# Performance work log

Hardware: AMD Instinct MI355X
Metric: run time of the kernel (lower is better)

Reference implementation:

```python
import jax, jax.numpy as jnp
import numpy as np

B, C, H, W = 16, 512, 64, 64
K = 4            # num_experts
D = C // 16      # reduction=16 -> hidden channels 32


def setup_inputs() -> dict:
    key = jax.random.key(0)
    ks = jax.random.split(key, 7)
    s_fc = 1.0 / np.sqrt(C)
    s_w1 = 1.0 / np.sqrt(C)   # conv1x1 fan_in = C
    s_w2 = 1.0 / np.sqrt(D)   # conv1x1 fan_in = D
    return {
        "x": jax.random.normal(ks[0], (B, C, H, W), dtype=jnp.float32),
        "fc_w": jax.random.uniform(ks[1], (K, C), minval=-s_fc, maxval=s_fc, dtype=jnp.float32),
        "fc_b": jax.random.uniform(ks[2], (K,), minval=-s_fc, maxval=s_fc, dtype=jnp.float32),
        "w1": jax.random.uniform(ks[3], (K, D, C), minval=-s_w1, maxval=s_w1, dtype=jnp.float32),
        "b1": jax.random.uniform(ks[4], (K, D), minval=-s_w1, maxval=s_w1, dtype=jnp.float32),
        "w2": jax.random.uniform(ks[5], (K, C, D), minval=-s_w2, maxval=s_w2, dtype=jnp.float32),
        "b2": jax.random.uniform(ks[6], (K, C), minval=-s_w2, maxval=s_w2, dtype=jnp.float32),
    }


def reference(x, fc_w, fc_b, w1, b1, w2, b2):
    # global average pool -> routing weights over K experts
    y = jnp.mean(x, axis=(2, 3))                                  # [B, C]
    weights = jax.nn.softmax(y @ fc_w.T + fc_b, axis=1)           # [B, K]
    # all experts' first conv1x1 + ReLU, batched over K
    hid = jax.nn.relu(
        jnp.einsum("bchw,kdc->bkdhw", x, w1) + b1[None, :, :, None, None]
    )                                                             # [B, K, D, H, W]
    # second conv1x1 fused with the weighted sum over experts (avoids [B,K,C,H,W])
    out = jnp.einsum("bkdhw,kcd,bk->bchw", hid, w2, weights)
    out = out + jnp.einsum("bk,kc->bc", weights, b2)[:, :, None, None]
    attn = jax.nn.sigmoid(out)                                    # [B, C, H, W]
    return x * attn
```

## Files before the change

kernel.cpp:

```cpp
#include <hip/hip_runtime.h>
#include <hip/hip_bf16.h>
#include <math.h>

#define BB 16
#define CC 512
#define HWN 4096
#define KK 4
#define DD 32
#define KD 128
#define NPIX 64

typedef __attribute__((ext_vector_type(8))) short short8;
typedef __attribute__((ext_vector_type(4))) float f32x4;

#define WS_Y     0
#define WS_WGT   8192
#define WS_BIAS2 8256
#define WS_W1B   16448
#define WS_W2B   49216

__device__ inline unsigned short f2bf(float f) {
    unsigned u = __builtin_bit_cast(unsigned, f);
    unsigned r = (u + 0x7FFFu + ((u >> 16) & 1u)) >> 16;
    return (unsigned short)r;
}

__global__ __launch_bounds__(256) void mean_kernel(const float* __restrict__ x,
                                                   float* __restrict__ y) {
    int wave = threadIdx.x >> 6;
    int lane = threadIdx.x & 63;
    int row  = blockIdx.x * 4 + wave;
    const float4* xr = (const float4*)(x + (size_t)row * HWN);
    float s = 0.f;
    #pragma unroll
    for (int i = 0; i < 16; i++) {
        float4 v = xr[i * 64 + lane];
        s += (v.x + v.y) + (v.z + v.w);
    }
    #pragma unroll
    for (int off = 32; off > 0; off >>= 1)
        s += __shfl_down(s, off, 64);
    if (lane == 0) y[row] = s * (1.0f / HWN);
}

__global__ __launch_bounds__(64) void route_kernel(const float* __restrict__ y,
                                                   const float* __restrict__ fc_w,
                                                   const float* __restrict__ fc_b,
                                                   float* __restrict__ wgt) {
    __shared__ float logits[BB][KK];
    int t = threadIdx.x;
    int b = t >> 2, k = t & 3;
    const float4* y4 = (const float4*)(y + b * CC);
    const float4* f4 = (const float4*)(fc_w + k * CC);
    float s = fc_b[k];
    for (int i = 0; i < CC / 4; i++) {
        float4 a = y4[i], w = f4[i];
        s += a.x * w.x + a.y * w.y + a.z * w.z + a.w * w.w;
    }
    logits[b][k] = s;
    __syncthreads();
    if (k == 0) {
        float m = logits[b][0];
        #pragma unroll
        for (int j = 1; j < KK; j++) m = fmaxf(m, logits[b][j]);
        float e[KK], sum = 0.f;
        #pragma unroll
        for (int j = 0; j < KK; j++) { e[j] = __expf(logits[b][j] - m); sum += e[j]; }
        float inv = 1.f / sum;
        #pragma unroll
        for (int j = 0; j < KK; j++) wgt[b * KK + j] = e[j] * inv;
    }
}

__global__ __launch_bounds__(256) void prep_kernel(const float* __restrict__ w1,
                                                   const float* __restrict__ w2,
                                                   const float* __restrict__ b2,
                                                   const float* __restrict__ wgt,
                                                   unsigned short* __restrict__ w1b,
                                                   unsigned short* __restrict__ w2b,
                                                   float* __restrict__ bias2) {
    int tid = blockIdx.x * 256 + threadIdx.x;
    int n   = gridDim.x * 256;
    for (int idx = tid; idx < CC * KD; idx += n) {
        int f = idx >> 9, rem = idx & 511;
        int l = rem >> 3, i = rem & 7;
        int ks = f >> 3, m = f & 7;
        int kd = m * 16 + (l & 15);
        int c  = ks * 32 + (l >> 4) * 8 + i;
        w1b[idx] = f2bf(w1[kd * CC + c]);
    }
    for (int idx = tid; idx < CC * KD; idx += n) {
        int f = idx >> 9, rem = idx & 511;
        int l = rem >> 3, i = rem & 7;
        int mc = f >> 2, kk = f & 3;
        int c = mc * 16 + (l & 15);
        int d = (l >> 4) * 8 + i;
        w2b[idx] = f2bf(w2[(kk * CC + c) * DD + d]);
    }
    for (int idx = tid; idx < BB * CC; idx += n) {
        int bb = idx >> 9, c = idx & 511;
        float s = 0.f;
        #pragma unroll
        for (int k = 0; k < KK; k++) s += wgt[bb * KK + k] * b2[k * CC + c];
        bias2[idx] = s;
    }
}

__global__ __launch_bounds__(512, 4) void main_kernel(const float* __restrict__ x,
                                                      const unsigned short* __restrict__ w1b,
                                                      const float* __restrict__ b1,
                                                      const unsigned short* __restrict__ w2b,
                                                      const float* __restrict__ wgt,
                                                      const float* __restrict__ bias2,
                                                      float* __restrict__ out) {
    __shared__ char lds[4 * 8192];

    const int b       = blockIdx.y;
    const int pixbase = blockIdx.x * NPIX;
    const int tid = threadIdx.x;
    const int wv  = tid >> 6;
    const int l   = tid & 63;
    const int l15 = l & 15, lg = l >> 4;
    const int pg  = wv & 3;
    const int kh  = wv >> 2;

    const float* xb = x + (size_t)b * CC * HWN;
    const short8* w1f = (const short8*)w1b;
    const short8* w2f = (const short8*)w2b;

    f32x4 acc1[8];
    #pragma unroll
    for (int m = 0; m < 8; m++) acc1[m] = (f32x4)0.f;

    const int mypix = pixbase + pg * 16 + l15;
    const float* xc = xb + (size_t)(kh * 256 + lg * 8) * HWN + mypix;

    float xv[8];
    #pragma unroll
    for (int i = 0; i < 8; i++) xv[i] = xc[(size_t)i * HWN];

    #pragma unroll
    for (int ks8 = 0; ks8 < 8; ks8++) {
        short8 bf;
        #pragma unroll
        for (int i = 0; i < 8; i++) bf[i] = (short)f2bf(xv[i]);
        if (ks8 < 7) {
            const float* xn = xc + (size_t)((ks8 + 1) * 32) * HWN;
            #pragma unroll
            for (int i = 0; i < 8; i++) xv[i] = xn[(size_t)i * HWN];
        }
        const int ks = kh * 8 + ks8;
        #pragma unroll
        for (int m = 0; m < 8; m++) {
            short8 af = w1f[(ks * 8 + m) * 64 + l];
            acc1[m] = __builtin_amdgcn_mfma_f32_16x16x32_bf16(af, bf, acc1[m], 0, 0, 0);
        }
    }

    if (kh == 1) {
        char* base = lds + pg * 8192 + lg * 256 + l15 * 16;
        #pragma unroll
        for (int m = 0; m < 8; m++)
            *(f32x4*)(base + m * 1024) = acc1[m];
    }
    __syncthreads();

    if (kh == 0) {
        const char* pbase = lds + pg * 8192 + lg * 256 + l15 * 16;
        #pragma unroll
        for (int half = 0; half < 2; half++) {
            f32x4 pp[4];
            #pragma unroll
            for (int m4 = 0; m4 < 4; m4++)
                pp[m4] = *(const f32x4*)(pbase + (half * 4 + m4) * 1024);
            #pragma unroll
            for (int m4 = 0; m4 < 4; m4++) {
                const int m = half * 4 + m4;
                f32x4 bv = *(const f32x4*)(b1 + m * 16 + lg * 4);
                float wk = wgt[b * KK + (m >> 1)];
                f32x4 s = acc1[m] + pp[m4];
                unsigned short h[4];
                #pragma unroll
                for (int r = 0; r < 4; r++) {
                    float t = fmaxf(s[r] + bv[r], 0.f) * wk;
                    h[r] = f2bf(t);
                }
                unsigned lo = (unsigned)h[0] | ((unsigned)h[1] << 16);
                unsigned hi = (unsigned)h[2] | ((unsigned)h[3] << 16);
                int byteoff = pg * 8192 + l15 * 256 + (m * 16 + lg * 4) * 2;
                byteoff ^= (l15 & 7) << 4;
                uint2 v; v.x = lo; v.y = hi;
                *(uint2*)(lds + byteoff) = v;
            }
        }
    }
    __syncthreads();

    const float* bb2 = bias2 + b * CC;
    #pragma unroll
    for (int mblk = 0; mblk < 4; mblk++) {
        f32x4 acc[4];
        #pragma unroll
        for (int nb = 0; nb < 4; nb++) acc[nb] = (f32x4)0.f;
        #pragma unroll
        for (int kk = 0; kk < 4; kk++) {
            short8 af = w2f[((wv * 4 + mblk) * 4 + kk) * 64 + l];
            #pragma unroll
            for (int nb = 0; nb < 4; nb++) {
                int byteoff = nb * 8192 + l15 * 256 + kk * 64 + lg * 16;
                byteoff ^= (l15 & 7) << 4;
                short8 bf = *(const short8*)(lds + byteoff);
                acc[nb] = __builtin_amdgcn_mfma_f32_16x16x32_bf16(af, bf, acc[nb], 0, 0, 0);
            }
        }
        const int cb = wv * 64 + mblk * 16 + lg * 4;
        f32x4 b2v = *(const f32x4*)(bb2 + cb);
        #pragma unroll
        for (int nb = 0; nb < 4; nb++) {
            int pix = pixbase + nb * 16 + l15;
            #pragma unroll
            for (int r = 0; r < 4; r++) {
                size_t off = ((size_t)b * CC + cb + r) * HWN + pix;
                float s = acc[nb][r] + b2v[r];
                float attn = __builtin_amdgcn_rcpf(1.f + __expf(-s));
                __builtin_nontemporal_store(x[off] * attn, &out[off]);
            }
        }
    }
}

extern "C" void kernel_launch(void* const* d_in, const int* in_sizes, int n_in,
                              void* d_out, int out_size, void* d_ws, size_t ws_size,
                              hipStream_t stream) {
    const float* x    = (const float*)d_in[0];
    const float* fc_w = (const float*)d_in[1];
    const float* fc_b = (const float*)d_in[2];
    const float* w1   = (const float*)d_in[3];
    const float* b1   = (const float*)d_in[4];
    const float* w2   = (const float*)d_in[5];
    const float* b2   = (const float*)d_in[6];
    float* out = (float*)d_out;
    float* ws  = (float*)d_ws;

    float* y     = ws + WS_Y;
    float* wgt   = ws + WS_WGT;
    float* bias2 = ws + WS_BIAS2;
    unsigned short* w1b = (unsigned short*)(ws + WS_W1B);
    unsigned short* w2b = (unsigned short*)(ws + WS_W2B);

    mean_kernel <<<dim3(BB * CC / 4), dim3(256), 0, stream>>>(x, y);
    route_kernel<<<dim3(1),           dim3(64),  0, stream>>>(y, fc_w, fc_b, wgt);
    prep_kernel <<<dim3(128),         dim3(256), 0, stream>>>(w1, w2, b2, wgt, w1b, w2b, bias2);
    main_kernel <<<dim3(HWN / NPIX, BB), dim3(512), 0, stream>>>(x, w1b, b1, w2b, wgt, bias2, out);
}
```

Measured before the change: 307.6 us.

## Pre-pack x into bf16 MFMA-fragment layout in a separate kernel

Adds a pack kernel that converts x to bf16 and stores it in the pixel-major, 32-channel-group layout that the MFMA B operand expects. The main kernel then loads each B fragment as one 16-byte vector instead of eight strided fp32 loads plus in-register conversion. The cost is an extra full pass over x: 128 MB read and 64 MB written to workspace, then read back. The main kernel still reads fp32 x later for the final multiply.

```diff
diff --git a/kernel.cpp b/kernel.cpp
--- a/kernel.cpp
+++ b/kernel.cpp
@@ -18,6 +18,7 @@
 #define WS_BIAS2 8256
 #define WS_W1B   16448
 #define WS_W2B   49216
+#define WS_XP    81984
 
 __device__ inline unsigned short f2bf(float f) {
     unsigned u = __builtin_bit_cast(unsigned, f);
@@ -41,6 +42,26 @@
     for (int off = 32; off > 0; off >>= 1)
         s += __shfl_down(s, off, 64);
     if (lane == 0) y[row] = s * (1.0f / HWN);
+}
+
+__global__ __launch_bounds__(256) void pack_kernel(const float* __restrict__ x,
+                                                   unsigned short* __restrict__ xp) {
+    const int b = blockIdx.z, ks = blockIdx.y;
+    const int pix = blockIdx.x * 256 + threadIdx.x;
+    const float* xc = x + (size_t)(b * CC + ks * 32) * HWN + pix;
+    unsigned u[16];
+    #pragma unroll
+    for (int c2 = 0; c2 < 16; c2++) {
+        float v0 = xc[(size_t)(2 * c2) * HWN];
+        float v1 = xc[(size_t)(2 * c2 + 1) * HWN];
+        u[c2] = (unsigned)f2bf(v0) | ((unsigned)f2bf(v1) << 16);
+    }
+    uint4* dst = (uint4*)(xp + ((size_t)(b * 16 + ks) * HWN + pix) * 32);
+    #pragma unroll
+    for (int q = 0; q < 4; q++) {
+        uint4 v; v.x = u[q*4]; v.y = u[q*4+1]; v.z = u[q*4+2]; v.w = u[q*4+3];
+        dst[q] = v;
+    }
 }
 
 __global__ __launch_bounds__(64) void route_kernel(const float* __restrict__ y,
@@ -107,6 +128,7 @@
 }
 
 __global__ __launch_bounds__(512, 4) void main_kernel(const float* __restrict__ x,
+                                                      const unsigned short* __restrict__ xp,
                                                       const unsigned short* __restrict__ w1b,
                                                       const float* __restrict__ b1,
                                                       const unsigned short* __restrict__ w2b,
@@ -124,36 +146,29 @@
     const int pg  = wv & 3;
     const int kh  = wv >> 2;
 
-    const float* xb = x + (size_t)b * CC * HWN;
     const short8* w1f = (const short8*)w1b;
     const short8* w2f = (const short8*)w2b;
+    const short8* xps = (const short8*)xp;
 
     f32x4 acc1[8];
     #pragma unroll
     for (int m = 0; m < 8; m++) acc1[m] = (f32x4)0.f;
 
     const int mypix = pixbase + pg * 16 + l15;
-    const float* xc = xb + (size_t)(kh * 256 + lg * 8) * HWN + mypix;
-
-    float xv[8];
-    #pragma unroll
-    for (int i = 0; i < 8; i++) xv[i] = xc[(size_t)i * HWN];
+    const size_t xbase = ((size_t)(b * 16 + kh * 8) * HWN + mypix) * 4 + lg;
+
+    short8 bfr[8];
+    #pragma unroll
+    for (int ks8 = 0; ks8 < 8; ks8++)
+        bfr[ks8] = xps[xbase + (size_t)ks8 * HWN * 4];
 
     #pragma unroll
     for (int ks8 = 0; ks8 < 8; ks8++) {
-        short8 bf;
-        #pragma unroll
-        for (int i = 0; i < 8; i++) bf[i] = (short)f2bf(xv[i]);
-        if (ks8 < 7) {
-            const float* xn = xc + (size_t)((ks8 + 1) * 32) * HWN;
-            #pragma unroll
-            for (int i = 0; i < 8; i++) xv[i] = xn[(size_t)i * HWN];
-        }
         const int ks = kh * 8 + ks8;
         #pragma unroll
         for (int m = 0; m < 8; m++) {
             short8 af = w1f[(ks * 8 + m) * 64 + l];
-            acc1[m] = __builtin_amdgcn_mfma_f32_16x16x32_bf16(af, bf, acc1[m], 0, 0, 0);
+            acc1[m] = __builtin_amdgcn_mfma_f32_16x16x32_bf16(af, bfr[ks8], acc1[m], 0, 0, 0);
         }
     }
 
@@ -247,9 +262,11 @@
     float* bias2 = ws + WS_BIAS2;
     unsigned short* w1b = (unsigned short*)(ws + WS_W1B);
     unsigned short* w2b = (unsigned short*)(ws + WS_W2B);
+    unsigned short* xp  = (unsigned short*)(ws + WS_XP);
 
     mean_kernel <<<dim3(BB * CC / 4), dim3(256), 0, stream>>>(x, y);
+    pack_kernel <<<dim3(HWN / 256, CC / 32, BB), dim3(256), 0, stream>>>(x, xp);
     route_kernel<<<dim3(1),           dim3(64),  0, stream>>>(y, fc_w, fc_b, wgt);
     prep_kernel <<<dim3(128),         dim3(256), 0, stream>>>(w1, w2, b2, wgt, w1b, w2b, bias2);
-    main_kernel <<<dim3(HWN / NPIX, BB), dim3(512), 0, stream>>>(x, w1b, b1, w2b, wgt, bias2, out);
-}
+    main_kernel <<<dim3(HWN / NPIX, BB), dim3(512), 0, stream>>>(x, xp, w1b, b1, w2b, wgt, bias2, out);
+}
```

Result: slower. 335.7 us (+9.1%).

## Stage x tile in LDS as bf16 and reuse it for the output multiply

Applied to the files above, without the earlier changes.

The main kernel now loads its whole 32-pixel by 512-channel x tile into LDS once, converted to bf16 with a swizzled layout. Both the first-conv MFMA operands and the final x*attn multiply read from that copy, so x is no longer fetched from global memory a second time. The block shrinks to 256 threads covering 32 pixels, and the second-conv B operands are held in registers. The trade-off is that the output multiply now uses bf16-rounded x instead of fp32 x, which adds output error, and LDS use grows to 48 KB per block, which can limit occupancy.

```diff
diff --git a/kernel.cpp b/kernel.cpp
--- a/kernel.cpp
+++ b/kernel.cpp
@@ -8,7 +8,7 @@
 #define KK 4
 #define DD 32
 #define KD 128
-#define NPIX 64
+#define NPIX 32
 
 typedef __attribute__((ext_vector_type(8))) short short8;
 typedef __attribute__((ext_vector_type(4))) float f32x4;
@@ -19,10 +19,16 @@
 #define WS_W1B   16448
 #define WS_W2B   49216
 
+#define PBASE 32768
+
 __device__ inline unsigned short f2bf(float f) {
     unsigned u = __builtin_bit_cast(unsigned, f);
     unsigned r = (u + 0x7FFFu + ((u >> 16) & 1u)) >> 16;
     return (unsigned short)r;
+}
+__device__ inline float bf2f(unsigned short h) {
+    unsigned u = (unsigned)h << 16;
+    return __builtin_bit_cast(float, u);
 }
 
 __global__ __launch_bounds__(256) void mean_kernel(const float* __restrict__ x,
@@ -106,14 +112,14 @@
     }
 }
 
-__global__ __launch_bounds__(512, 4) void main_kernel(const float* __restrict__ x,
+__global__ __launch_bounds__(256, 3) void main_kernel(const float* __restrict__ x,
                                                       const unsigned short* __restrict__ w1b,
                                                       const float* __restrict__ b1,
                                                       const unsigned short* __restrict__ w2b,
                                                       const float* __restrict__ wgt,
                                                       const float* __restrict__ bias2,
                                                       float* __restrict__ out) {
-    __shared__ char lds[4 * 8192];
+    __shared__ char lds[49152];
 
     const int b       = blockIdx.y;
     const int pixbase = blockIdx.x * NPIX;
@@ -121,44 +127,64 @@
     const int wv  = tid >> 6;
     const int l   = tid & 63;
     const int l15 = l & 15, lg = l >> 4;
-    const int pg  = wv & 3;
-    const int kh  = wv >> 2;
-
-    const float* xb = x + (size_t)b * CC * HWN;
+    const int pg  = wv & 1;
+    const int kh  = wv >> 1;
+
     const short8* w1f = (const short8*)w1b;
     const short8* w2f = (const short8*)w2b;
 
+    {
+        const int apix = tid & 31;
+        const int ag   = tid >> 5;
+        const float* xb = x + (size_t)b * CC * HWN + pixbase + apix;
+        float v[8][8];
+        #pragma unroll
+        for (int i = 0; i < 8; i++) {
+            const int cb = i * 64 + ag * 8;
+            #pragma unroll
+            for (int j = 0; j < 8; j++)
+                v[i][j] = xb[(size_t)(cb + j) * HWN];
+        }
+        const int sw = (apix & 15) << 4;
+        #pragma unroll
+        for (int i = 0; i < 8; i++) {
+            const int cb = i * 64 + ag * 8;
+            uint4 p;
+            p.x = (unsigned)f2bf(v[i][0]) | ((unsigned)f2bf(v[i][1]) << 16);
+            p.y = (unsigned)f2bf(v[i][2]) | ((unsigned)f2bf(v[i][3]) << 16);
+            p.z = (unsigned)f2bf(v[i][4]) | ((unsigned)f2bf(v[i][5]) << 16);
+            p.w = (unsigned)f2bf(v[i][6]) | ((unsigned)f2bf(v[i][7]) << 16);
+            *(uint4*)(lds + apix * 1024 + ((cb * 2) ^ sw)) = p;
+        }
+    }
+    __syncthreads();
+
     f32x4 acc1[8];
     #pragma unroll
     for (int m = 0; m < 8; m++) acc1[m] = (f32x4)0.f;
 
-    const int mypix = pixbase + pg * 16 + l15;
-    const float* xc = xb + (size_t)(kh * 256 + lg * 8) * HWN + mypix;
-
-    float xv[8];
-    #pragma unroll
-    for (int i = 0; i < 8; i++) xv[i] = xc[(size_t)i * HWN];
-
-    #pragma unroll
-    for (int ks8 = 0; ks8 < 8; ks8++) {
-        short8 bf;
-        #pragma unroll
-        for (int i = 0; i < 8; i++) bf[i] = (short)f2bf(xv[i]);
-        if (ks8 < 7) {
-            const float* xn = xc + (size_t)((ks8 + 1) * 32) * HWN;
-            #pragma unroll
-            for (int i = 0; i < 8; i++) xv[i] = xn[(size_t)i * HWN];
-        }
-        const int ks = kh * 8 + ks8;
-        #pragma unroll
-        for (int m = 0; m < 8; m++) {
-            short8 af = w1f[(ks * 8 + m) * 64 + l];
-            acc1[m] = __builtin_amdgcn_mfma_f32_16x16x32_bf16(af, bf, acc1[m], 0, 0, 0);
+    {
+        const int mp  = pg * 16 + l15;
+        const int msw = (mp & 15) << 4;
+        short8 bfr[8];
+        #pragma unroll
+        for (int ks8 = 0; ks8 < 8; ks8++) {
+            const int c0 = (kh * 8 + ks8) * 32 + lg * 8;
+            bfr[ks8] = *(const short8*)(lds + mp * 1024 + ((c0 * 2) ^ msw));
+        }
+        #pragma unroll
+        for (int ks8 = 0; ks8 < 8; ks8++) {
+            const int ks = kh * 8 + ks8;
+            #pragma unroll
+            for (int m = 0; m < 8; m++) {
+                short8 af = w1f[(ks * 8 + m) * 64 + l];
+                acc1[m] = __builtin_amdgcn_mfma_f32_16x16x32_bf16(af, bfr[ks8], acc1[m], 0, 0, 0);
+            }
         }
     }
 
     if (kh == 1) {
-        char* base = lds + pg * 8192 + lg * 256 + l15 * 16;
+        char* base = lds + PBASE + pg * 8192 + lg * 256 + l15 * 16;
         #pragma unroll
         for (int m = 0; m < 8; m++)
             *(f32x4*)(base + m * 1024) = acc1[m];
@@ -166,7 +192,7 @@
     __syncthreads();
 
     if (kh == 0) {
-        const char* pbase = lds + pg * 8192 + lg * 256 + l15 * 16;
+        const char* pbase = lds + PBASE + pg * 8192 + lg * 256 + l15 * 16;
         #pragma unroll
         for (int half = 0; half < 2; half++) {
             f32x4 pp[4];
@@ -187,8 +213,7 @@
                 }
                 unsigned lo = (unsigned)h[0] | ((unsigned)h[1] << 16);
                 unsigned hi = (unsigned)h[2] | ((unsigned)h[3] << 16);
-                int byteoff = pg * 8192 + l15 * 256 + (m * 16 + lg * 4) * 2;
-                byteoff ^= (l15 & 7) << 4;
+                int byteoff = PBASE + pg * 8192 + l15 * 256 + (((m * 16 + lg * 4) * 2) ^ ((l15 & 7) << 4));
                 uint2 v; v.x = lo; v.y = hi;
                 *(uint2*)(lds + byteoff) = v;
             }
@@ -196,34 +221,44 @@
     }
     __syncthreads();
 
+    short8 breg[4][2];
+    #pragma unroll
+    for (int kk = 0; kk < 4; kk++)
+        #pragma unroll
+        for (int nb = 0; nb < 2; nb++)
+            breg[kk][nb] = *(const short8*)(lds + PBASE + nb * 8192 + l15 * 256 +
+                                            (((kk * 64 + lg * 16)) ^ ((l15 & 7) << 4)));
+
     const float* bb2 = bias2 + b * CC;
     #pragma unroll
-    for (int mblk = 0; mblk < 4; mblk++) {
-        f32x4 acc[4];
-        #pragma unroll
-        for (int nb = 0; nb < 4; nb++) acc[nb] = (f32x4)0.f;
+    for (int mblk = 0; mblk < 8; mblk++) {
+        f32x4 acc[2];
+        acc[0] = (f32x4)0.f; acc[1] = (f32x4)0.f;
         #pragma unroll
         for (int kk = 0; kk < 4; kk++) {
-            short8 af = w2f[((wv * 4 + mblk) * 4 + kk) * 64 + l];
-            #pragma unroll
-            for (int nb = 0; nb < 4; nb++) {
-                int byteoff = nb * 8192 + l15 * 256 + kk * 64 + lg * 16;
-                byteoff ^= (l15 & 7) << 4;
-                short8 bf = *(const short8*)(lds + byteoff);
-                acc[nb] = __builtin_amdgcn_mfma_f32_16x16x32_bf16(af, bf, acc[nb], 0, 0, 0);
-            }
-        }
-        const int cb = wv * 64 + mblk * 16 + lg * 4;
+            short8 af = w2f[((wv * 8 + mblk) * 4 + kk) * 64 + l];
+            #pragma unroll
+            for (int nb = 0; nb < 2; nb++)
+                acc[nb] = __builtin_amdgcn_mfma_f32_16x16x32_bf16(af, breg[kk][nb], acc[nb], 0, 0, 0);
+        }
+        const int cb = wv * 128 + mblk * 16 + lg * 4;
         f32x4 b2v = *(const f32x4*)(bb2 + cb);
         #pragma unroll
-        for (int nb = 0; nb < 4; nb++) {
-            int pix = pixbase + nb * 16 + l15;
+        for (int nb = 0; nb < 2; nb++) {
+            const int pixl = nb * 16 + l15;
+            uint2 xw = *(const uint2*)(lds + pixl * 1024 + ((cb * 2) ^ ((pixl & 15) << 4)));
+            float xr[4];
+            xr[0] = bf2f((unsigned short)(xw.x & 0xFFFF));
+            xr[1] = bf2f((unsigned short)(xw.x >> 16));
+            xr[2] = bf2f((unsigned short)(xw.y & 0xFFFF));
+            xr[3] = bf2f((unsigned short)(xw.y >> 16));
+            const int pix = pixbase + pixl;
             #pragma unroll
             for (int r = 0; r < 4; r++) {
                 size_t off = ((size_t)b * CC + cb + r) * HWN + pix;
                 float s = acc[nb][r] + b2v[r];
                 float attn = __builtin_amdgcn_rcpf(1.f + __expf(-s));
-                __builtin_nontemporal_store(x[off] * attn, &out[off]);
+                __builtin_nontemporal_store(xr[r] * attn, &out[off]);
             }
         }
     }
@@ -251,5 +286,5 @@
     mean_kernel <<<dim3(BB * CC / 4), dim3(256), 0, stream>>>(x, y);
     route_kernel<<<dim3(1),           dim3(64),  0, stream>>>(y, fc_w, fc_b, wgt);
     prep_kernel <<<dim3(128),         dim3(256), 0, stream>>>(w1, w2, b2, wgt, w1b, w2b, bias2);
-    main_kernel <<<dim3(HWN / NPIX, BB), dim3(512), 0, stream>>>(x, w1b, b1, w2b, wgt, bias2, out);
-}
+    main_kernel <<<dim3(HWN / NPIX, BB), dim3(256), 0, stream>>>(x, w1b, b1, w2b, wgt, bias2, out);
+}
```

After: 303.1 us. Within noise of the previous version (-1.5%).
